# Performance work log

Hardware: AMD Instinct MI355X
Metric: run time of the kernel (lower is better)

## Reference

```python
import jax, jax.numpy as jnp
import numpy as np

EMBED_DIM = 1024
NUM_HEADS = 16
HEAD_DIM = EMBED_DIM // NUM_HEADS
FF_DIM = 4096
LN_EPS = 1e-5


def layer_norm(x, scale, bias):
    mu = jnp.mean(x, axis=-1, keepdims=True)
    var = jnp.mean(jnp.square(x - mu), axis=-1, keepdims=True)
    return (x - mu) * jax.lax.rsqrt(var + LN_EPS) * scale + bias


def setup_inputs() -> dict:
    key = jax.random.key(0)
    ks = jax.random.split(key, 9)
    E, F = EMBED_DIM, FF_DIM
    s = lambda d: 1.0 / np.sqrt(d)
    return {
        "x": jax.random.normal(ks[0], (2, 2048, E), dtype=jnp.float32),
        "qkv_w": jax.random.uniform(ks[1], (3 * E, E), jnp.float32, -s(E), s(E)),
        "out_w": jax.random.uniform(ks[2], (E, E), jnp.float32, -s(E), s(E)),
        "ff_up_w": jax.random.uniform(ks[3], (F, E), jnp.float32, -s(E), s(E)),
        "ff_down_w": jax.random.uniform(ks[4], (E, F), jnp.float32, -s(F), s(F)),
        "norm1_scale": jnp.ones((E,), jnp.float32),
        "norm1_bias": jnp.zeros((E,), jnp.float32),
        "norm2_scale": jnp.ones((E,), jnp.float32),
        "norm2_bias": jnp.zeros((E,), jnp.float32),
    }


def reference(x, qkv_w, out_w, ff_up_w, ff_down_w,
              norm1_scale, norm1_bias, norm2_scale, norm2_bias):
    B, S, E = x.shape
    H, D = NUM_HEADS, HEAD_DIM

    # --- attention sublayer ---
    residual = x
    h = layer_norm(x, norm1_scale, norm1_bias)
    qkv = h @ qkv_w.T                               # [B,S,3E]
    qkv = qkv.reshape(B, S, 3, H, D).transpose(2, 0, 3, 1, 4)  # [3,B,H,S,D]
    q, k, v = qkv[0], qkv[1], qkv[2]
    scores = jnp.einsum("bhqd,bhkd->bhqk", q, k) / np.sqrt(D)
    probs = jax.nn.softmax(scores, axis=-1)
    attn = jnp.einsum("bhqk,bhkd->bhqd", probs, v)  # [B,H,S,D]
    attn = attn.transpose(0, 2, 1, 3).reshape(B, S, E)
    x = residual + attn @ out_w.T

    # --- FFN sublayer ---
    residual = x
    h = layer_norm(x, norm2_scale, norm2_bias)
    h = jax.nn.gelu(h @ ff_up_w.T, approximate=False)
    h = h @ ff_down_w.T
    return residual + h
```

## Files before the change

### kernel.cpp

```cpp
#include <hip/hip_runtime.h>

typedef unsigned short u16;
typedef unsigned int u32;
typedef __attribute__((ext_vector_type(8))) short bf16x8;
typedef __attribute__((ext_vector_type(4))) float f32x4;

#define MFMA_BF16(a, b, c) __builtin_amdgcn_mfma_f32_16x16x32_bf16((a), (b), (c), 0, 0, 0)
#define BAR() __builtin_amdgcn_s_barrier()
#define WAITV(n) asm volatile("s_waitcnt vmcnt(" #n ")" ::: "memory")

#if __has_builtin(__builtin_amdgcn_exp2f)
#define EXP2(x) __builtin_amdgcn_exp2f(x)
#else
#define EXP2(x) exp2f(x)
#endif

__device__ __forceinline__ u16 f2bf(float f) {
    u32 u = __builtin_bit_cast(u32, f);
    u32 r = u + 0x7FFFu + ((u >> 16) & 1u);
    return (u16)(r >> 16);
}

__device__ __forceinline__ void gld16(const void* g, void* s) {
    __builtin_amdgcn_global_load_lds(
        (const __attribute__((address_space(1))) unsigned int*)g,
        (__attribute__((address_space(3))) unsigned int*)s, 16, 0, 0);
}

__global__ __launch_bounds__(256) void cvtall_k(const float* __restrict__ w0,
                                                const float* __restrict__ w1,
                                                const float* __restrict__ w2,
                                                const float* __restrict__ w3,
                                                u16* o0, u16* o1, u16* o2, u16* o3) {
    int j = blockIdx.x * 256 + threadIdx.x;
    const float* src; u16* dst;
    if (j < 786432)                       { src = w0; dst = o0; }
    else if ((j -= 786432) < 262144)      { src = w1; dst = o1; }
    else if ((j -= 262144) < 1048576)     { src = w2; dst = o2; }
    else { j -= 1048576;                    src = w3; dst = o3; }
    float4 v = ((const float4*)src)[j];
    ushort4 o;
    o.x = f2bf(v.x); o.y = f2bf(v.y); o.z = f2bf(v.z); o.w = f2bf(v.w);
    ((ushort4*)dst)[j] = o;
}

__global__ __launch_bounds__(256) void ln_k(const float* __restrict__ x,
                                            u16* __restrict__ out,
                                            const float* __restrict__ sc,
                                            const float* __restrict__ bi) {
    const int row = blockIdx.x;
    const int tid = threadIdx.x;
    const float4 v = ((const float4*)(x + (size_t)row * 1024))[tid];
    float s  = v.x + v.y + v.z + v.w;
    float s2 = v.x*v.x + v.y*v.y + v.z*v.z + v.w*v.w;
    #pragma unroll
    for (int m = 32; m; m >>= 1) { s += __shfl_xor(s, m); s2 += __shfl_xor(s2, m); }
    __shared__ float red[8];
    const int w = tid >> 6, l = tid & 63;
    if (l == 0) { red[w] = s; red[4 + w] = s2; }
    __syncthreads();
    s  = red[0] + red[1] + red[2] + red[3];
    s2 = red[4] + red[5] + red[6] + red[7];
    const float mu  = s * (1.0f / 1024.0f);
    const float var = s2 * (1.0f / 1024.0f) - mu * mu;
    const float rs  = rsqrtf(var + 1e-5f);
    const float4 sv = ((const float4*)sc)[tid];
    const float4 bv = ((const float4*)bi)[tid];
    ushort4 o;
    o.x = f2bf((v.x - mu) * rs * sv.x + bv.x);
    o.y = f2bf((v.y - mu) * rs * sv.y + bv.y);
    o.z = f2bf((v.z - mu) * rs * sv.z + bv.z);
    o.w = f2bf((v.w - mu) * rs * sv.w + bv.w);
    ((ushort4*)(out + (size_t)row * 1024))[tid] = o;
}

template<int NT, int EPI>
__global__ __launch_bounds__(512, 1) void gemm256_k(const u16* __restrict__ A,
                                                    const u16* __restrict__ B,
                                                    u16* __restrict__ Cb,
                                                    u16* __restrict__ vtout,
                                                    int M, int N, int K) {
    extern __shared__ u16 L[];
    const int tid = threadIdx.x;
    const int w = tid >> 6, l = tid & 63, g = l >> 4, lc = l & 15;
    const int wr = w >> 2, wc = w & 3;

    const int gx = gridDim.x, gy = gridDim.y;
    const int lin = blockIdx.x + gx * blockIdx.y;
    const int rx = gx >> 2, cy = gy >> 1;
    const int xcd = lin & 7, slot = lin >> 3;
    const int brow = (xcd & 3) * rx + (slot % rx);
    const int bcol = (xcd >> 2) * cy + (slot / rx);
    const int row0 = brow * 256, col0 = bcol * 256;

    const u16* gA = A + (size_t)row0 * K;
    const u16* gB = B + (size_t)col0 * K;
    int srow[4], soct[4];
    #pragma unroll
    for (int p = 0; p < 4; ++p) {
        const int idx = p * 512 + tid;
        srow[p] = idx >> 3;
        soct[p] = (idx & 7) ^ (srow[p] & 7);
    }

#define STG(t, p) do { \
        char* base_ = (char*)L + ((t) & 1) * 65536; \
        gld16(gA + (size_t)srow[p] * K + (size_t)(t) * 64 + soct[p] * 8, \
              base_ + ((p) * 512 + tid) * 16); \
        gld16(gB + (size_t)srow[p] * K + (size_t)(t) * 64 + soct[p] * 8, \
              base_ + 32768 + ((p) * 512 + tid) * 16); \
    } while (0)

    f32x4 acc[8][4] = {};

    STG(0, 0); STG(0, 1); STG(0, 2); STG(0, 3);

    const int ocx = lc & 7;

    for (int t = 0; t < NT; ++t) {
        const bool pf = (t + 1 < NT);
        if (pf) { STG(t + 1, 0); WAITV(2); } else { WAITV(0); }
        BAR();

        const u16* La = L + (t & 1) * 32768;
        const u16* Lb = La + 16384;

        bf16x8 bfr[4][2];
        #pragma unroll
        for (int j = 0; j < 4; ++j)
            #pragma unroll
            for (int kk = 0; kk < 2; ++kk)
                bfr[j][kk] = *(const bf16x8*)
                    &Lb[(wc * 64 + j * 16 + lc) * 64 + (((kk * 4 + g) ^ ocx) * 8)];

        #pragma unroll
        for (int ph = 0; ph < 4; ++ph) {
            if (ph == 2) BAR();
            bf16x8 af[2][2];
            #pragma unroll
            for (int ii = 0; ii < 2; ++ii)
                #pragma unroll
                for (int kk = 0; kk < 2; ++kk)
                    af[ii][kk] = *(const bf16x8*)
                        &La[(wr * 128 + (ph * 2 + ii) * 16 + lc) * 64 +
                            (((kk * 4 + g) ^ ocx) * 8)];
            __builtin_amdgcn_s_setprio(1);
            #pragma unroll
            for (int ii = 0; ii < 2; ++ii)
                #pragma unroll
                for (int j = 0; j < 4; ++j)
                    #pragma unroll
                    for (int kk = 0; kk < 2; ++kk)
                        acc[ph * 2 + ii][j] = MFMA_BF16(af[ii][kk], bfr[j][kk],
                                                        acc[ph * 2 + ii][j]);
            __builtin_amdgcn_s_setprio(0);
            if (pf && ph < 3) STG(t + 1, ph + 1);
        }
    }
#undef STG

    #pragma unroll
    for (int i = 0; i < 8; ++i)
        #pragma unroll
        for (int j = 0; j < 4; ++j) {
            const int rowb = row0 + wr * 128 + i * 16 + g * 4;
            const int col  = col0 + wc * 64 + j * 16 + lc;
            if (EPI == 0 && col >= 2048) {
                u32 lo, hi;
                asm("v_cvt_pk_bf16_f32 %0, %1, %2"
                    : "=v"(lo) : "v"(acc[i][j][0]), "v"(acc[i][j][1]));
                asm("v_cvt_pk_bf16_f32 %0, %1, %2"
                    : "=v"(hi) : "v"(acc[i][j][2]), "v"(acc[i][j][3]));
                const int hd = col - 2048, bb = rowb >> 11, token = rowb & 2047;
                uint2 pk; pk.x = lo; pk.y = hi;
                *(uint2*)(vtout + ((size_t)(bb * 16 + (hd >> 6)) * 64 + (hd & 63)) * 2048
                          + token) = pk;
            } else {
                #pragma unroll
                for (int r = 0; r < 4; ++r) {
                    const size_t off = (size_t)(rowb + r) * N + col;
                    const float v = acc[i][j][r];
                    if (EPI == 0) {
                        const float vv = (col < 1024) ? v * 0.180336880f : v;
                        Cb[off] = f2bf(vv);
                    } else {
                        const float u2 = fminf((v + 0.044715f * v * v * v)
                                               * 2.302118131f, 126.0f);
                        const float e = EXP2(u2);
                        Cb[off] = f2bf(v * e / (e + 1.0f));
                    }
                }
            }
        }
}

template<int NT>
__global__ __launch_bounds__(512, 1) void gemm128w8_k(const u16* __restrict__ A,
                                                      const u16* __restrict__ B,
                                                      float* __restrict__ Cf,
                                                      const float* __restrict__ resid,
                                                      int M, int N, int K) {
    extern __shared__ u16 L[];
    const int tid = threadIdx.x;
    const int w = tid >> 6, l = tid & 63, g = l >> 4, lc = l & 15;
    const int wr = w >> 1, wc = w & 1;
    const int row0 = blockIdx.x * 128, col0 = blockIdx.y * 128;

    const u16* gA = A + (size_t)row0 * K;
    const u16* gB = B + (size_t)col0 * K;
    const int srow = tid >> 3;
    const int soct = (tid & 7) ^ (srow & 7);

#define STG8(t) do { \
        char* base_ = (char*)L + ((t) & 3) * 32768; \
        _Pragma("unroll") \
        for (int p = 0; p < 4; ++p) { \
            const u16* src_ = (p < 2) ? gB : gA; \
            const int row_ = ((p & 1) << 6) + srow; \
            gld16(src_ + (size_t)row_ * K + (size_t)(t) * 64 + soct * 8, \
                  base_ + p * 8192 + tid * 16); \
        } \
    } while (0)

    f32x4 acc[2][4] = {};

    STG8(0); STG8(1); STG8(2);

    const int ocx = lc & 7;

    for (int t = 0; t < NT; ++t) {
        if      (t + 2 < NT) WAITV(8);
        else if (t + 1 < NT) WAITV(4);
        else                 WAITV(0);
        BAR();
        if (t + 3 < NT) STG8(t + 3);

        const u16* Lb = L + (t & 3) * 16384;
        const u16* La = Lb + 8192;

        bf16x8 bfr[4][2], af[2][2];
        #pragma unroll
        for (int j = 0; j < 4; ++j)
            #pragma unroll
            for (int kk = 0; kk < 2; ++kk)
                bfr[j][kk] = *(const bf16x8*)
                    &Lb[(wc * 64 + j * 16 + lc) * 64 + (((kk * 4 + g) ^ ocx) * 8)];
        #pragma unroll
        for (int ii = 0; ii < 2; ++ii)
            #pragma unroll
            for (int kk = 0; kk < 2; ++kk)
                af[ii][kk] = *(const bf16x8*)
                    &La[(wr * 32 + ii * 16 + lc) * 64 + (((kk * 4 + g) ^ ocx) * 8)];

        __builtin_amdgcn_s_setprio(1);
        #pragma unroll
        for (int ii = 0; ii < 2; ++ii)
            #pragma unroll
            for (int j = 0; j < 4; ++j)
                #pragma unroll
                for (int kk = 0; kk < 2; ++kk)
                    acc[ii][j] = MFMA_BF16(af[ii][kk], bfr[j][kk], acc[ii][j]);
        __builtin_amdgcn_s_setprio(0);
    }
#undef STG8

    #pragma unroll
    for (int i = 0; i < 2; ++i)
        #pragma unroll
        for (int j = 0; j < 4; ++j)
            #pragma unroll
            for (int r = 0; r < 4; ++r) {
                const int row = row0 + wr * 32 + i * 16 + g * 4 + r;
                const int col = col0 + wc * 64 + j * 16 + lc;
                const size_t off = (size_t)row * N + col;
                Cf[off] = acc[i][j][r] + resid[off];
            }
}

__global__ __launch_bounds__(512) void attn_k(const u16* __restrict__ qkv,
                                              const u16* __restrict__ vt,
                                              u16* __restrict__ ctx) {
    const int bh = blockIdx.x;
    const int qt = blockIdx.y;
    const int b = bh >> 4, h = bh & 15;
    const int tid = threadIdx.x, w = tid >> 6, l = tid & 63, g = l >> 4, lc = l & 15;
    const size_t tok0 = (size_t)b * 2048;

    const u16* Qg  = qkv + (tok0 + qt * 128) * 3072 + h * 64;
    const u16* Kg  = qkv + tok0 * 3072 + 1024 + h * 64;
    const u16* Vtg = vt + (size_t)bh * 64 * 2048;

    __shared__ u16 Ks[3][64 * 64];
    __shared__ u16 Vts[3][64 * 64];
    __shared__ u16 QPs[128 * 64];
    u16* Pw = QPs + w * 1024;

    {
        const int q0r = tid >> 3,         q0c = (tid & 7) ^ (q0r & 7);
        const int q1r = (tid + 512) >> 3, q1c = ((tid + 512) & 7) ^ (q1r & 7);
        gld16(Qg + (size_t)q0r * 3072 + q0c * 8, (char*)QPs + tid * 16);
        gld16(Qg + (size_t)q1r * 3072 + q1c * 8, (char*)QPs + (tid + 512) * 16);
    }
    const int skr = tid >> 3, skc = (tid & 7) ^ (skr & 7);
    const u16* kp = Kg + (size_t)skr * 3072 + skc * 8;
    const u16* vp = Vtg + (size_t)skr * 2048 + skc * 8;
    gld16(kp, (char*)Ks[0] + tid * 16);
    gld16(vp, (char*)Vts[0] + tid * 16);
    kp += 64 * 3072; vp += 64;
    gld16(kp, (char*)Ks[1] + tid * 16);
    gld16(vp, (char*)Vts[1] + tid * 16);
    kp += 64 * 3072; vp += 64;
    __syncthreads();

    bf16x8 qf[2];
    {
        const int qrow = w * 16 + lc;
        qf[0] = *(const bf16x8*)&QPs[qrow * 64 + ((g       ^ (lc & 7)) * 8)];
        qf[1] = *(const bf16x8*)&QPs[qrow * 64 + (((4 + g) ^ (lc & 7)) * 8)];
    }

    f32x4 oacc[4] = {};
    float mrow = -1e30f, lrow = 0.0f;
    const int hsw = (lc & 7) << 3;

    int cs = 0, ss = 2;
    for (int kt = 0; kt < 32; ++kt) {
        if (kt + 1 < 32) { WAITV(2); } else { WAITV(0); }
        BAR();
        if (kt + 2 < 32) {
            gld16(kp, (char*)Ks[ss] + tid * 16);
            gld16(vp, (char*)Vts[ss] + tid * 16);
            kp += 64 * 3072; vp += 64;
        }
        const u16* Kc = Ks[cs];
        const u16* Vc = Vts[cs];
        cs = (cs == 2) ? 0 : cs + 1;
        ss = (ss == 2) ? 0 : ss + 1;

        f32x4 sacc[4] = {};
        __builtin_amdgcn_s_setprio(1);
        #pragma unroll
        for (int kk = 0; kk < 2; ++kk)
            #pragma unroll
            for (int nt = 0; nt < 4; ++nt) {
                const int krow = nt * 16 + lc;
                const bf16x8 kb = *(const bf16x8*)
                    &Kc[krow * 64 + (((kk * 4 + g) ^ (lc & 7)) * 8)];
                sacc[nt] = MFMA_BF16(kb, qf[kk], sacc[nt]);
            }
        __builtin_amdgcn_s_setprio(0);

        float mx;
        {
            const float* sv = (const float*)sacc;
            float m = sv[0];
            #pragma unroll
            for (int q = 0; q < 7; ++q) {
                float t;
                asm("v_max3_f32 %0, %1, %2, %3"
                    : "=v"(t) : "v"(m), "v"(sv[2 * q + 1]), "v"(sv[2 * q + 2]));
                m = t;
            }
            mx = fmaxf(m, sv[15]);
        }
        mx = fmaxf(mx, __shfl_xor(mx, 16));
        mx = fmaxf(mx, __shfl_xor(mx, 32));
        const bool ru = __any(mx > mrow + 8.0f);
        float corr = 1.0f;
        if (ru) {
            const float mnew = fmaxf(mrow, mx);
            corr = EXP2(mrow - mnew);
            mrow = mnew;
        }

        float p[4][4];
        float ps = 0.0f;
        #pragma unroll
        for (int nt = 0; nt < 4; ++nt)
            #pragma unroll
            for (int r = 0; r < 4; ++r) {
                const float pv = EXP2(sacc[nt][r] - mrow);
                p[nt][r] = pv;
                ps += pv;
            }
        ps += __shfl_xor(ps, 16);
        ps += __shfl_xor(ps, 32);

        #pragma unroll
        for (int nt = 0; nt < 4; ++nt) {
            uint2 pk;
            asm("v_cvt_pk_bf16_f32 %0, %1, %2" : "=v"(pk.x) : "v"(p[nt][0]), "v"(p[nt][1]));
            asm("v_cvt_pk_bf16_f32 %0, %1, %2" : "=v"(pk.y) : "v"(p[nt][2]), "v"(p[nt][3]));
            *(uint2*)&Pw[lc * 64 + ((nt * 16 + g * 4) ^ hsw)] = pk;
        }

        if (ru) {
            lrow = lrow * corr + ps;
            float cq[4];
            #pragma unroll
            for (int r = 0; r < 4; ++r) cq[r] = __shfl(corr, g * 4 + r);
            #pragma unroll
            for (int nt = 0; nt < 4; ++nt)
                #pragma unroll
                for (int r = 0; r < 4; ++r) oacc[nt][r] *= cq[r];
        } else {
            lrow += ps;
        }

        __builtin_amdgcn_s_setprio(1);
        #pragma unroll
        for (int kk = 0; kk < 2; ++kk) {
            const bf16x8 pa = *(const bf16x8*)
                &Pw[lc * 64 + ((kk * 32 + g * 8) ^ hsw)];
            #pragma unroll
            for (int nt = 0; nt < 4; ++nt) {
                const int vrow = nt * 16 + lc;
                const bf16x8 vb = *(const bf16x8*)
                    &Vc[vrow * 64 + (((kk * 4 + g) ^ (lc & 7)) * 8)];
                oacc[nt] = MFMA_BF16(pa, vb, oacc[nt]);
            }
        }
        __builtin_amdgcn_s_setprio(0);
    }

    float lq[4];
    #pragma unroll
    for (int r = 0; r < 4; ++r) lq[r] = 1.0f / __shfl(lrow, g * 4 + r);
    #pragma unroll
    for (int nt = 0; nt < 4; ++nt)
        #pragma unroll
        for (int r = 0; r < 4; ++r) {
            const float o = oacc[nt][r] * lq[r];
            const size_t token = tok0 + qt * 128 + w * 16 + g * 4 + r;
            ctx[token * 1024 + h * 64 + nt * 16 + lc] = f2bf(o);
        }
}

extern "C" void kernel_launch(void* const* d_in, const int* in_sizes, int n_in,
                              void* d_out, int out_size, void* d_ws, size_t ws_size,
                              hipStream_t stream) {
    const float* x      = (const float*)d_in[0];
    const float* qkv_w  = (const float*)d_in[1];
    const float* out_w  = (const float*)d_in[2];
    const float* up_w   = (const float*)d_in[3];
    const float* down_w = (const float*)d_in[4];
    const float* n1s    = (const float*)d_in[5];
    const float* n1b    = (const float*)d_in[6];
    const float* n2s    = (const float*)d_in[7];
    const float* n2b    = (const float*)d_in[8];
    float* out = (float*)d_out;

    char* ws = (char*)d_ws;
    size_t off = 0;
    auto alloc = [&](size_t bytes) -> void* {
        void* p = ws + off;
        off += (bytes + 255) & ~(size_t)255;
        return p;
    };
    u16*   qkvw_b = (u16*)alloc(3072ull * 1024 * 2);
    u16*   outw_b = (u16*)alloc(1024ull * 1024 * 2);
    u16*   upw_b  = (u16*)alloc(4096ull * 1024 * 2);
    u16*   dnw_b  = (u16*)alloc(1024ull * 4096 * 2);
    u16*   h_b    = (u16*)alloc(4096ull * 1024 * 2);
    u16*   qkv_o  = (u16*)alloc(4096ull * 3072 * 2);
    u16*   ctx    = (u16*)alloc(4096ull * 1024 * 2);
    float* x2     = (float*)alloc(4096ull * 1024 * 4);
    u16*   u      = (u16*)alloc(4096ull * 4096 * 2);
    u16*   vt     = u;

    hipFuncSetAttribute((const void*)&gemm256_k<16, 0>,
                        hipFuncAttributeMaxDynamicSharedMemorySize, 131072);
    hipFuncSetAttribute((const void*)&gemm256_k<16, 2>,
                        hipFuncAttributeMaxDynamicSharedMemorySize, 131072);
    hipFuncSetAttribute((const void*)&gemm128w8_k<16>,
                        hipFuncAttributeMaxDynamicSharedMemorySize, 131072);
    hipFuncSetAttribute((const void*)&gemm128w8_k<64>,
                        hipFuncAttributeMaxDynamicSharedMemorySize, 131072);

    cvtall_k<<<12288, 256, 0, stream>>>(qkv_w, out_w, up_w, down_w,
                                        qkvw_b, outw_b, upw_b, dnw_b);

    ln_k<<<4096, 256, 0, stream>>>(x, h_b, n1s, n1b);
    gemm256_k<16, 0><<<dim3(16, 12), 512, 131072, stream>>>(h_b, qkvw_b, qkv_o, vt,
                                                            4096, 3072, 1024);
    attn_k<<<dim3(32, 16), 512, 0, stream>>>(qkv_o, vt, ctx);
    gemm128w8_k<16><<<dim3(32, 8), 512, 131072, stream>>>(ctx, outw_b, x2, x,
                                                          4096, 1024, 1024);

    ln_k<<<4096, 256, 0, stream>>>(x2, h_b, n2s, n2b);
    gemm256_k<16, 2><<<dim3(16, 16), 512, 131072, stream>>>(h_b, upw_b, u, nullptr,
                                                            4096, 4096, 1024);
    gemm128w8_k<64><<<dim3(32, 8), 512, 131072, stream>>>(u, dnw_b, out, x2,
                                                          4096, 1024, 4096);
}
```

Measured before the change: 205.6 us.

## Process 256 queries per attention block with two 16-row subtiles per wave

Each attention block now handles 256 query rows instead of 128, with every wave owning two 16-row query subtiles that share each K and V fragment loaded from LDS. This halves the number of K/V tile loads from global memory per head and doubles MFMA work per LDS read. In exchange, the grid shrinks from 512 to 256 blocks, which may underfill the GPU's compute units, and register pressure and LDS usage (Q/P buffer doubles to 32KB) rise.

After: 213.4 us. 3.8% more time.

```diff
diff --git a/kernel.cpp b/kernel.cpp
--- a/kernel.cpp
+++ b/kernel.cpp
@@ -286,20 +286,20 @@
     const int tid = threadIdx.x, w = tid >> 6, l = tid & 63, g = l >> 4, lc = l & 15;
     const size_t tok0 = (size_t)b * 2048;
 
-    const u16* Qg  = qkv + (tok0 + qt * 128) * 3072 + h * 64;
+    const u16* Qg  = qkv + (tok0 + qt * 256) * 3072 + h * 64;
     const u16* Kg  = qkv + tok0 * 3072 + 1024 + h * 64;
     const u16* Vtg = vt + (size_t)bh * 64 * 2048;
 
     __shared__ u16 Ks[3][64 * 64];
     __shared__ u16 Vts[3][64 * 64];
-    __shared__ u16 QPs[128 * 64];
-    u16* Pw = QPs + w * 1024;
-
-    {
-        const int q0r = tid >> 3,         q0c = (tid & 7) ^ (q0r & 7);
-        const int q1r = (tid + 512) >> 3, q1c = ((tid + 512) & 7) ^ (q1r & 7);
-        gld16(Qg + (size_t)q0r * 3072 + q0c * 8, (char*)QPs + tid * 16);
-        gld16(Qg + (size_t)q1r * 3072 + q1c * 8, (char*)QPs + (tid + 512) * 16);
+    __shared__ u16 QPs[256 * 64];
+    u16* Pw = QPs + w * 2048;
+
+    #pragma unroll
+    for (int c = 0; c < 4; ++c) {
+        const int idx = c * 512 + tid;
+        const int qr = idx >> 3, qc = (idx & 7) ^ (qr & 7);
+        gld16(Qg + (size_t)qr * 3072 + qc * 8, (char*)QPs + idx * 16);
     }
     const int skr = tid >> 3, skc = (tid & 7) ^ (skr & 7);
     const u16* kp = Kg + (size_t)skr * 3072 + skc * 8;
@@ -312,15 +312,16 @@
     kp += 64 * 3072; vp += 64;
     __syncthreads();
 
-    bf16x8 qf[2];
-    {
-        const int qrow = w * 16 + lc;
-        qf[0] = *(const bf16x8*)&QPs[qrow * 64 + ((g       ^ (lc & 7)) * 8)];
-        qf[1] = *(const bf16x8*)&QPs[qrow * 64 + (((4 + g) ^ (lc & 7)) * 8)];
-    }
-
-    f32x4 oacc[4] = {};
-    float mrow = -1e30f, lrow = 0.0f;
+    bf16x8 qf[2][2];
+    #pragma unroll
+    for (int s = 0; s < 2; ++s) {
+        const int qrow = w * 32 + s * 16 + lc;
+        qf[s][0] = *(const bf16x8*)&QPs[qrow * 64 + ((g       ^ (lc & 7)) * 8)];
+        qf[s][1] = *(const bf16x8*)&QPs[qrow * 64 + (((4 + g) ^ (lc & 7)) * 8)];
+    }
+
+    f32x4 oacc[2][4] = {};
+    float mrow[2] = {-1e30f, -1e30f}, lrow[2] = {0.0f, 0.0f};
     const int hsw = (lc & 7) << 3;
 
     int cs = 0, ss = 2;
@@ -337,7 +338,7 @@
         cs = (cs == 2) ? 0 : cs + 1;
         ss = (ss == 2) ? 0 : ss + 1;
 
-        f32x4 sacc[4] = {};
+        f32x4 sacc[2][4] = {};
         __builtin_amdgcn_s_setprio(1);
         #pragma unroll
         for (int kk = 0; kk < 2; ++kk)
@@ -346,94 +347,106 @@
                 const int krow = nt * 16 + lc;
                 const bf16x8 kb = *(const bf16x8*)
                     &Kc[krow * 64 + (((kk * 4 + g) ^ (lc & 7)) * 8)];
-                sacc[nt] = MFMA_BF16(kb, qf[kk], sacc[nt]);
+                sacc[0][nt] = MFMA_BF16(kb, qf[0][kk], sacc[0][nt]);
+                sacc[1][nt] = MFMA_BF16(kb, qf[1][kk], sacc[1][nt]);
             }
         __builtin_amdgcn_s_setprio(0);
 
-        float mx;
-        {
-            const float* sv = (const float*)sacc;
-            float m = sv[0];
-            #pragma unroll
-            for (int q = 0; q < 7; ++q) {
-                float t;
-                asm("v_max3_f32 %0, %1, %2, %3"
-                    : "=v"(t) : "v"(m), "v"(sv[2 * q + 1]), "v"(sv[2 * q + 2]));
-                m = t;
-            }
-            mx = fmaxf(m, sv[15]);
+        #pragma unroll
+        for (int s = 0; s < 2; ++s) {
+            float mx;
+            {
+                const float* sv = (const float*)sacc[s];
+                float m = sv[0];
+                #pragma unroll
+                for (int q = 0; q < 7; ++q) {
+                    float t;
+                    asm("v_max3_f32 %0, %1, %2, %3"
+                        : "=v"(t) : "v"(m), "v"(sv[2 * q + 1]), "v"(sv[2 * q + 2]));
+                    m = t;
+                }
+                mx = fmaxf(m, sv[15]);
+            }
+            mx = fmaxf(mx, __shfl_xor(mx, 16));
+            mx = fmaxf(mx, __shfl_xor(mx, 32));
+            const bool ru = __any(mx > mrow[s] + 8.0f);
+            float corr = 1.0f;
+            if (ru) {
+                const float mnew = fmaxf(mrow[s], mx);
+                corr = EXP2(mrow[s] - mnew);
+                mrow[s] = mnew;
+            }
+
+            float p[4][4];
+            float ps = 0.0f;
+            #pragma unroll
+            for (int nt = 0; nt < 4; ++nt)
+                #pragma unroll
+                for (int r = 0; r < 4; ++r) {
+                    const float pv = EXP2(sacc[s][nt][r] - mrow[s]);
+                    p[nt][r] = pv;
+                    ps += pv;
+                }
+            ps += __shfl_xor(ps, 16);
+            ps += __shfl_xor(ps, 32);
+
+            #pragma unroll
+            for (int nt = 0; nt < 4; ++nt) {
+                uint2 pk;
+                asm("v_cvt_pk_bf16_f32 %0, %1, %2"
+                    : "=v"(pk.x) : "v"(p[nt][0]), "v"(p[nt][1]));
+                asm("v_cvt_pk_bf16_f32 %0, %1, %2"
+                    : "=v"(pk.y) : "v"(p[nt][2]), "v"(p[nt][3]));
+                *(uint2*)&Pw[(s * 16 + lc) * 64 + ((nt * 16 + g * 4) ^ hsw)] = pk;
+            }
+
+            if (ru) {
+                lrow[s] = lrow[s] * corr + ps;
+                float cq[4];
+                #pragma unroll
+                for (int r = 0; r < 4; ++r) cq[r] = __shfl(corr, g * 4 + r);
+                #pragma unroll
+                for (int nt = 0; nt < 4; ++nt)
+                    #pragma unroll
+                    for (int r = 0; r < 4; ++r) oacc[s][nt][r] *= cq[r];
+            } else {
+                lrow[s] += ps;
+            }
         }
-        mx = fmaxf(mx, __shfl_xor(mx, 16));
-        mx = fmaxf(mx, __shfl_xor(mx, 32));
-        const bool ru = __any(mx > mrow + 8.0f);
-        float corr = 1.0f;
-        if (ru) {
-            const float mnew = fmaxf(mrow, mx);
-            corr = EXP2(mrow - mnew);
-            mrow = mnew;
-        }
-
-        float p[4][4];
-        float ps = 0.0f;
-        #pragma unroll
-        for (int nt = 0; nt < 4; ++nt)
-            #pragma unroll
-            for (int r = 0; r < 4; ++r) {
-                const float pv = EXP2(sacc[nt][r] - mrow);
-                p[nt][r] = pv;
-                ps += pv;
-            }
-        ps += __shfl_xor(ps, 16);
-        ps += __shfl_xor(ps, 32);
-
-        #pragma unroll
-        for (int nt = 0; nt < 4; ++nt) {
-            uint2 pk;
-            asm("v_cvt_pk_bf16_f32 %0, %1, %2" : "=v"(pk.x) : "v"(p[nt][0]), "v"(p[nt][1]));
-            asm("v_cvt_pk_bf16_f32 %0, %1, %2" : "=v"(pk.y) : "v"(p[nt][2]), "v"(p[nt][3]));
-            *(uint2*)&Pw[lc * 64 + ((nt * 16 + g * 4) ^ hsw)] = pk;
-        }
-
-        if (ru) {
-            lrow = lrow * corr + ps;
-            float cq[4];
-            #pragma unroll
-            for (int r = 0; r < 4; ++r) cq[r] = __shfl(corr, g * 4 + r);
-            #pragma unroll
-            for (int nt = 0; nt < 4; ++nt)
-                #pragma unroll
-                for (int r = 0; r < 4; ++r) oacc[nt][r] *= cq[r];
-        } else {
-            lrow += ps;
-        }
 
         __builtin_amdgcn_s_setprio(1);
         #pragma unroll
         for (int kk = 0; kk < 2; ++kk) {
-            const bf16x8 pa = *(const bf16x8*)
+            const bf16x8 pa0 = *(const bf16x8*)
                 &Pw[lc * 64 + ((kk * 32 + g * 8) ^ hsw)];
+            const bf16x8 pa1 = *(const bf16x8*)
+                &Pw[(16 + lc) * 64 + ((kk * 32 + g * 8) ^ hsw)];
             #pragma unroll
             for (int nt = 0; nt < 4; ++nt) {
                 const int vrow = nt * 16 + lc;
                 const bf16x8 vb = *(const bf16x8*)
                     &Vc[vrow * 64 + (((kk * 4 + g) ^ (lc & 7)) * 8)];
-                oacc[nt] = MFMA_BF16(pa, vb, oacc[nt]);
+                oacc[0][nt] = MFMA_BF16(pa0, vb, oacc[0][nt]);
+                oacc[1][nt] = MFMA_BF16(pa1, vb, oacc[1][nt]);
             }
         }
         __builtin_amdgcn_s_setprio(0);
     }
 
-    float lq[4];
-    #pragma unroll
-    for (int r = 0; r < 4; ++r) lq[r] = 1.0f / __shfl(lrow, g * 4 + r);
-    #pragma unroll
-    for (int nt = 0; nt < 4; ++nt)
-        #pragma unroll
-        for (int r = 0; r < 4; ++r) {
-            const float o = oacc[nt][r] * lq[r];
-            const size_t token = tok0 + qt * 128 + w * 16 + g * 4 + r;
-            ctx[token * 1024 + h * 64 + nt * 16 + lc] = f2bf(o);
-        }
+    #pragma unroll
+    for (int s = 0; s < 2; ++s) {
+        float lq[4];
+        #pragma unroll
+        for (int r = 0; r < 4; ++r) lq[r] = 1.0f / __shfl(lrow[s], g * 4 + r);
+        #pragma unroll
+        for (int nt = 0; nt < 4; ++nt)
+            #pragma unroll
+            for (int r = 0; r < 4; ++r) {
+                const float o = oacc[s][nt][r] * lq[r];
+                const size_t token = tok0 + qt * 256 + w * 32 + s * 16 + g * 4 + r;
+                ctx[token * 1024 + h * 64 + nt * 16 + lc] = f2bf(o);
+            }
+    }
 }
 
 extern "C" void kernel_launch(void* const* d_in, const int* in_sizes, int n_in,
@@ -483,7 +496,7 @@
     ln_k<<<4096, 256, 0, stream>>>(x, h_b, n1s, n1b);
     gemm256_k<16, 0><<<dim3(16, 12), 512, 131072, stream>>>(h_b, qkvw_b, qkv_o, vt,
                                                             4096, 3072, 1024);
-    attn_k<<<dim3(32, 16), 512, 0, stream>>>(qkv_o, vt, ctx);
+    attn_k<<<dim3(32, 8), 512, 0, stream>>>(qkv_o, vt, ctx);
     gemm128w8_k<16><<<dim3(32, 8), 512, 131072, stream>>>(ctx, outw_b, x2, x,
                                                           4096, 1024, 1024);
 
```
